# Kernel tuning notes

Measured on AMD Instinct MI355X. Metric: run time of the kernel, lower is better.

Reference implementation:

```python
import jax, jax.numpy as jnp
import numpy as np

N_NODES = 100000
N_EDGES = 1600000
IN_DIM, H1, H2, N_CLASSES = 128, 64, 64, 16
NEG_SLOPE = 0.2  # PyG GATConv default leaky_relu slope


def _xavier(key, shape, gain=1.414):
    fan_in, fan_out = shape[0], shape[-1]
    a = gain * np.sqrt(6.0 / (fan_in + fan_out))
    return jax.random.uniform(key, shape, jnp.float32, -a, a)


def setup_inputs() -> dict:
    key = jax.random.key(0)
    ks = jax.random.split(key, 12)
    ft_list = jax.random.normal(ks[0], (N_NODES, IN_DIM), jnp.float32)
    adj_tensor = jax.random.randint(ks[1], (2, N_EDGES), 0, N_NODES, jnp.int64)
    return {
        "ft_list": ft_list,
        "adj_tensor": adj_tensor,
        "W1": _xavier(ks[2], (IN_DIM, H1)),
        "a_src1": _xavier(ks[3], (H1, 1))[:, 0],
        "a_dst1": _xavier(ks[4], (H1, 1))[:, 0],
        "b1": jnp.zeros((H1,), jnp.float32),
        "W2": _xavier(ks[5], (H1, H2)),
        "a_src2": _xavier(ks[6], (H2, 1))[:, 0],
        "a_dst2": _xavier(ks[7], (H2, 1))[:, 0],
        "b2": jnp.zeros((H2,), jnp.float32),
        "clas_W": _xavier(ks[8], (H2, N_CLASSES)),
        "clas_b": _xavier(ks[9], (1, N_CLASSES)),
    }


def _gat_conv(x, src, dst, n, W, a_src, a_dst, b):
    # h: [N, H] transformed node features
    h = x @ W
    alpha_s = h @ a_src  # [N]
    alpha_d = h @ a_dst  # [N]
    # per-edge attention logit (gather)
    e = jax.nn.leaky_relu(alpha_s[src] + alpha_d[dst], NEG_SLOPE)  # [E]
    # segment softmax over edges grouped by destination node
    m = jax.ops.segment_max(e, dst, num_segments=n)
    p = jnp.exp(e - m[dst])
    s = jax.ops.segment_sum(p, dst, num_segments=n)
    attn = p / s[dst]  # [E]
    # weighted scatter-add of source features
    out = jax.ops.segment_sum(h[src] * attn[:, None], dst, num_segments=n)
    return out + b


def reference(ft_list, adj_tensor, W1, a_src1, a_dst1, b1, W2, a_src2, a_dst2, b2, clas_W, clas_b):
    n = ft_list.shape[0]
    loop = jnp.arange(n, dtype=adj_tensor.dtype)
    src = jnp.concatenate([adj_tensor[0], loop])  # add self-loops (PyG default)
    dst = jnp.concatenate([adj_tensor[1], loop])
    x = _gat_conv(ft_list, src, dst, n, W1, a_src1, a_dst1, b1)
    x = jax.nn.elu(x)
    # dropout(0.5) is identity in eval mode
    x = _gat_conv(x, src, dst, n, W2, a_src2, a_dst2, b2)
    logits = x @ clas_W + clas_b
    return logits, x
```

## Files before the change

### kernel.cpp

```cpp
#include <hip/hip_runtime.h>
#include <hip/hip_bf16.h>

#define NEG_SLOPE 0.2f
#define LOG2E 1.4426950408889634f
#define BSH 9
#define BW  (1 << BSH)
#define CH  4096
#define PGRID 256

typedef short short8 __attribute__((ext_vector_type(8)));
typedef float f32x4 __attribute__((ext_vector_type(4)));


__global__ __launch_bounds__(256) void bucket_hist_kernel(
    const int* __restrict__ adj, int* __restrict__ H, int E, int N, int R, int NBK)
{
    __shared__ int hist[256];
    const int t = threadIdx.x;
    const int ET = E + N;
    for (int r = blockIdx.x; r < R; r += gridDim.x) {
        hist[t] = 0;
        __syncthreads();
        int base = r * CH;
        for (int i = 0; i < CH / 256; ++i) {
            int e = base + i * 256 + t;
            if (e >= ET) break;
            int d = (e < E) ? adj[E + e] : (e - E);
            atomicAdd(&hist[d >> BSH], 1);
        }
        __syncthreads();
        if (t < NBK) H[r * NBK + t] = hist[t];
        __syncthreads();
    }
}

__global__ __launch_bounds__(256) void scan_rounds_kernel(
    const int* __restrict__ H, int* __restrict__ S2, int* __restrict__ tot,
    int R, int NBK)
{
    __shared__ int part[256];
    const int b = blockIdx.x;
    const int t = threadIdx.x;
    const int C = (R + 255) / 256;
    int r0 = t * C, r1 = min(R, r0 + C);
    int s = 0;
    for (int r = r0; r < r1; ++r) s += H[r * NBK + b];
    part[t] = s;
    __syncthreads();
    for (int off = 1; off < 256; off <<= 1) {
        int v = (t >= off) ? part[t - off] : 0;
        __syncthreads();
        part[t] += v;
        __syncthreads();
    }
    int run = (t > 0) ? part[t - 1] : 0;
    for (int r = r0; r < r1; ++r) {
        int h = H[r * NBK + b];
        S2[r * NBK + b] = run;
        run += h;
    }
    if (t == 255) tot[b] = part[255];
}

__global__ __launch_bounds__(256) void scan_tot_kernel(
    const int* __restrict__ tot, int* __restrict__ base, int NBK)
{
    __shared__ int s[256];
    int t = threadIdx.x;
    int v = (t < NBK) ? tot[t] : 0;
    s[t] = v;
    __syncthreads();
    for (int off = 1; off < 256; off <<= 1) {
        int u = (t >= off) ? s[t - off] : 0;
        __syncthreads();
        s[t] += u;
        __syncthreads();
    }
    if (t < NBK) base[t] = s[t] - v;
}

__global__ __launch_bounds__(256) void partition_kernel(
    const int* __restrict__ adj, const int* __restrict__ S2,
    const int* __restrict__ base, int* __restrict__ pbuf,
    int E, int N, int R, int NBK)
{
    __shared__ int lcur[256];
    const int t = threadIdx.x;
    const int ET = E + N;
    for (int r = blockIdx.x; r < R; r += gridDim.x) {
        if (t < NBK) lcur[t] = base[t] + S2[r * NBK + t];
        __syncthreads();
        int b0 = r * CH;
        for (int i = 0; i < CH / 256; ++i) {
            int e = b0 + i * 256 + t;
            if (e >= ET) break;
            int s, d;
            if (e < E) { d = adj[E + e]; s = adj[e]; }
            else       { s = d = e - E; }
            int b = d >> BSH;
            int pos = atomicAdd(&lcur[b], 1);
            pbuf[pos] = (s << BSH) | (d & (BW - 1));
        }
        __syncthreads();
    }
}

__global__ __launch_bounds__(256) void csr_build_kernel(
    const int* __restrict__ base, const int* __restrict__ tot,
    const int* __restrict__ pbuf,
    int* __restrict__ row_ptr, int* __restrict__ col_idx, int E, int N, int NBK)
{
    __shared__ int offA[BW];
    __shared__ int lcur[BW];
    const int b = blockIdx.x;
    const int t = threadIdx.x;
    const int node0 = b << BSH;
    const int nn = min(BW, N - node0);
    const int ET = E + N;
    const int segbeg = base[b];
    const int segend = segbeg + tot[b];

    offA[t] = 0; offA[t + 256] = 0;
    __syncthreads();
    for (int i = segbeg + t; i < segend; i += 256)
        atomicAdd(&offA[pbuf[i] & (BW - 1)], 1);
    __syncthreads();
    for (int off = 1; off < BW; off <<= 1) {
        int i1 = t + 256;
        int v0 = (t >= off) ? offA[t - off] : 0;
        int v1 = (i1 >= off) ? offA[i1 - off] : 0;
        __syncthreads();
        offA[t] += v0; offA[i1] += v1;
        __syncthreads();
    }
    if (t < nn) {
        int ex = t ? offA[t - 1] : 0;
        row_ptr[node0 + t] = segbeg + ex;
        lcur[t] = segbeg + ex;
    }
    int i2 = t + 256;
    if (i2 < nn) {
        int ex = offA[i2 - 1];
        row_ptr[node0 + i2] = segbeg + ex;
        lcur[i2] = segbeg + ex;
    }
    if (b == NBK - 1 && t == 0) row_ptr[N] = ET;
    __syncthreads();
    for (int i = segbeg + t; i < segend; i += 256) {
        int p = pbuf[i];
        int pos = atomicAdd(&lcur[p & (BW - 1)], 1);
        col_idx[pos] = p >> BSH;
    }
}


__device__ __forceinline__ unsigned short f2bf(float f)
{
    union { __hip_bfloat16 b; unsigned short u; } v;
    v.b = __float2bfloat16(f);
    return v.u;
}

__global__ __launch_bounds__(256) void prep_wfrag_kernel(
    const float* __restrict__ W, unsigned short* __restrict__ wf, int K)
{
    int total = K * 64;
    int idx = blockIdx.x * 256 + threadIdx.x;
    if (idx >= total) return;
    int i = idx & 7;
    int l = (idx >> 3) & 63;
    int f = idx >> 9;
    int s = f >> 2, tt = f & 3;
    int k = 32 * s + 8 * (l >> 4) + i;
    int n = 16 * tt + (l & 15);
    wf[idx] = f2bf(W[k * 64 + n]);
}

template<int K>
__global__ __launch_bounds__(256) void gemm_alpha_mfma(
    const float* __restrict__ X, const unsigned short* __restrict__ wf,
    const float* __restrict__ a_src, const float* __restrict__ a_dst,
    __hip_bfloat16* __restrict__ h, float* __restrict__ as_, float* __restrict__ ad_,
    int N, int nChunks)
{
    constexpr int S = K / 32;
    const int t = threadIdx.x;
    const int wave = t >> 6, lane = t & 63;
    const int g = lane >> 4, c = lane & 15;

    short8 bf[S * 4];
#pragma unroll
    for (int f = 0; f < S * 4; ++f)
        bf[f] = *(const short8*)(wf + ((size_t)(f * 64 + lane)) * 8);

    float asr[4], adr[4];
#pragma unroll
    for (int tt = 0; tt < 4; ++tt) {
        asr[tt] = a_src[16 * tt + c];
        adr[tt] = a_dst[16 * tt + c];
    }

    for (int chunk = blockIdx.x; chunk < nChunks; chunk += gridDim.x) {
        const int r0 = chunk * 64 + wave * 16;
        const int arow = r0 + c;
        const bool rv = arow < N;
        const float* xr = X + (size_t)arow * K;

        f32x4 acc[4];
#pragma unroll
        for (int tt = 0; tt < 4; ++tt) acc[tt] = (f32x4){0.f, 0.f, 0.f, 0.f};

#pragma unroll
        for (int s = 0; s < S; ++s) {
            float4 x0 = make_float4(0.f, 0.f, 0.f, 0.f);
            float4 x1 = make_float4(0.f, 0.f, 0.f, 0.f);
            if (rv) {
                const float4* p = (const float4*)(xr + 32 * s + 8 * g);
                x0 = p[0]; x1 = p[1];
            }
            float xs[8] = {x0.x, x0.y, x0.z, x0.w, x1.x, x1.y, x1.z, x1.w};
            union { short8 v; unsigned u[4]; } ah, al;
#pragma unroll
            for (int p2 = 0; p2 < 4; ++p2) {
                unsigned u0 = __float_as_uint(xs[2 * p2]);
                unsigned u1 = __float_as_uint(xs[2 * p2 + 1]);
                ah.u[p2] = (u0 >> 16) | (u1 & 0xffff0000u);
                float h0 = __uint_as_float(u0 & 0xffff0000u);
                float h1 = __uint_as_float(u1 & 0xffff0000u);
                unsigned l0 = __float_as_uint(xs[2 * p2] - h0);
                unsigned l1 = __float_as_uint(xs[2 * p2 + 1] - h1);
                al.u[p2] = (l0 >> 16) | (l1 & 0xffff0000u);
            }
#pragma unroll
            for (int tt = 0; tt < 4; ++tt) {
                acc[tt] = __builtin_amdgcn_mfma_f32_16x16x32_bf16(
                    ah.v, bf[s * 4 + tt], acc[tt], 0, 0, 0);
                acc[tt] = __builtin_amdgcn_mfma_f32_16x16x32_bf16(
                    al.v, bf[s * 4 + tt], acc[tt], 0, 0, 0);
            }
        }

#pragma unroll
        for (int i = 0; i < 4; ++i) {
            const int ri = r0 + 4 * g + i;
            float va = 0.f, vd = 0.f;
#pragma unroll
            for (int tt = 0; tt < 4; ++tt) {
                float v = acc[tt][i];
                va += v * asr[tt];
                vd += v * adr[tt];
                if (ri < N) h[(size_t)ri * 64 + 16 * tt + c] = __float2bfloat16(v);
            }
#pragma unroll
            for (int off = 8; off >= 1; off >>= 1) {
                va += __shfl_xor(va, off, 16);
                vd += __shfl_xor(vd, off, 16);
            }
            if (c == 0 && ri < N) { as_[ri] = va * LOG2E; ad_[ri] = vd * LOG2E; }
        }
    }
}

__global__ __launch_bounds__(256) void gat_aggregate_kernel(
    const int* __restrict__ row_ptr, const int* __restrict__ col_idx,
    const float* __restrict__ as_, const float* __restrict__ ad_,
    const __hip_bfloat16* __restrict__ h, const float* __restrict__ b,
    float* __restrict__ out, int N, int do_elu)
{
    int node = blockIdx.x * 4 + (threadIdx.x >> 6);
    int lane = threadIdx.x & 63;
    int sub = lane >> 3, q = lane & 7;
    if (node >= N) return;
    int beg = row_ptr[node], end = row_ptr[node + 1];
    float ad = ad_[node];
    float acc[8] = {0.f, 0.f, 0.f, 0.f, 0.f, 0.f, 0.f, 0.f};
    float psum = 0.f;

    const char* cbp = (const char*)col_idx;
    const char* abp = (const char*)as_;
    const char* hbp = (const char*)h;
    const unsigned qb = (unsigned)q * 16u;

    int base = beg;
    unsigned co = (unsigned)(beg + sub) * 4u;
    for (; base + 16 <= end; base += 16, co += 64u) {
        int s0 = *(const int*)(cbp + co);
        int s1 = *(const int*)(cbp + (co + 32u));
        float x0 = *(const float*)(abp + ((unsigned)s0 << 2)) + ad;
        float x1 = *(const float*)(abp + ((unsigned)s1 << 2)) + ad;
        uint4 u0 = *(const uint4*)(hbp + (((unsigned)s0 << 7) + qb));
        uint4 u1 = *(const uint4*)(hbp + (((unsigned)s1 << 7) + qb));
        x0 = fmaxf(x0, NEG_SLOPE * x0);
        x1 = fmaxf(x1, NEG_SLOPE * x1);
        float p0 = __builtin_amdgcn_exp2f(x0);
        float p1 = __builtin_amdgcn_exp2f(x1);
        psum += p0 + p1;
        unsigned w;
        w = u0.x; acc[0] += p0 * __uint_as_float(w << 16); acc[1] += p0 * __uint_as_float(w & 0xffff0000u);
        w = u0.y; acc[2] += p0 * __uint_as_float(w << 16); acc[3] += p0 * __uint_as_float(w & 0xffff0000u);
        w = u0.z; acc[4] += p0 * __uint_as_float(w << 16); acc[5] += p0 * __uint_as_float(w & 0xffff0000u);
        w = u0.w; acc[6] += p0 * __uint_as_float(w << 16); acc[7] += p0 * __uint_as_float(w & 0xffff0000u);
        w = u1.x; acc[0] += p1 * __uint_as_float(w << 16); acc[1] += p1 * __uint_as_float(w & 0xffff0000u);
        w = u1.y; acc[2] += p1 * __uint_as_float(w << 16); acc[3] += p1 * __uint_as_float(w & 0xffff0000u);
        w = u1.z; acc[4] += p1 * __uint_as_float(w << 16); acc[5] += p1 * __uint_as_float(w & 0xffff0000u);
        w = u1.w; acc[6] += p1 * __uint_as_float(w << 16); acc[7] += p1 * __uint_as_float(w & 0xffff0000u);
    }
    for (; base < end; base += 8, co += 32u) {
        int e0 = base + sub;
        bool v0 = e0 < end;
        unsigned c0 = (unsigned)(v0 ? e0 : end - 1) * 4u;
        int s0 = *(const int*)(cbp + c0);
        float x0 = *(const float*)(abp + ((unsigned)s0 << 2)) + ad;
        uint4 u0 = *(const uint4*)(hbp + (((unsigned)s0 << 7) + qb));
        x0 = fmaxf(x0, NEG_SLOPE * x0);
        float p0 = v0 ? __builtin_amdgcn_exp2f(x0) : 0.f;
        psum += p0;
        unsigned w;
        w = u0.x; acc[0] += p0 * __uint_as_float(w << 16); acc[1] += p0 * __uint_as_float(w & 0xffff0000u);
        w = u0.y; acc[2] += p0 * __uint_as_float(w << 16); acc[3] += p0 * __uint_as_float(w & 0xffff0000u);
        w = u0.z; acc[4] += p0 * __uint_as_float(w << 16); acc[5] += p0 * __uint_as_float(w & 0xffff0000u);
        w = u0.w; acc[6] += p0 * __uint_as_float(w << 16); acc[7] += p0 * __uint_as_float(w & 0xffff0000u);
    }
#pragma unroll
    for (int off = 8; off <= 32; off <<= 1) {
        psum += __shfl_xor(psum, off, 64);
#pragma unroll
        for (int j = 0; j < 8; ++j) acc[j] += __shfl_xor(acc[j], off, 64);
    }
    if (sub == 0) {
        float inv = 1.f / psum;
        const float* bq = b + q * 8;
        float4 b0 = *(const float4*)bq;
        float4 b1 = *(const float4*)(bq + 4);
        float v[8];
        v[0] = acc[0] * inv + b0.x; v[1] = acc[1] * inv + b0.y;
        v[2] = acc[2] * inv + b0.z; v[3] = acc[3] * inv + b0.w;
        v[4] = acc[4] * inv + b1.x; v[5] = acc[5] * inv + b1.y;
        v[6] = acc[6] * inv + b1.z; v[7] = acc[7] * inv + b1.w;
        if (do_elu) {
#pragma unroll
            for (int j = 0; j < 8; ++j)
                v[j] = v[j] > 0.f ? v[j] : (__expf(v[j]) - 1.f);
        }
        float* op = out + (size_t)node * 64 + q * 8;
        ((float4*)op)[0] = make_float4(v[0], v[1], v[2], v[3]);
        ((float4*)op)[1] = make_float4(v[4], v[5], v[6], v[7]);
    }
}

__global__ __launch_bounds__(256) void classifier_kernel(
    const float* __restrict__ x, const float* __restrict__ cw,
    const float* __restrict__ cb, float* __restrict__ out, int N)
{
    int i = blockIdx.x * blockDim.x + threadIdx.x;
    if (i >= N * 16) return;
    int n = i >> 4, c = i & 15;
    const float4* xr = (const float4*)(x + (size_t)n * 64);
    float acc = cb[c];
#pragma unroll
    for (int j4 = 0; j4 < 16; ++j4) {
        float4 xv = xr[j4];
        acc += xv.x * cw[(j4 * 4 + 0) * 16 + c];
        acc += xv.y * cw[(j4 * 4 + 1) * 16 + c];
        acc += xv.z * cw[(j4 * 4 + 2) * 16 + c];
        acc += xv.w * cw[(j4 * 4 + 3) * 16 + c];
    }
    out[i] = acc;
}

extern "C" void kernel_launch(void* const* d_in, const int* in_sizes, int n_in,
                              void* d_out, int out_size, void* d_ws, size_t ws_size,
                              hipStream_t stream)
{
    const float* X    = (const float*)d_in[0];
    const int*   adj  = (const int*)d_in[1];
    const float* W1   = (const float*)d_in[2];
    const float* a_s1 = (const float*)d_in[3];
    const float* a_d1 = (const float*)d_in[4];
    const float* b1   = (const float*)d_in[5];
    const float* W2   = (const float*)d_in[6];
    const float* a_s2 = (const float*)d_in[7];
    const float* a_d2 = (const float*)d_in[8];
    const float* b2   = (const float*)d_in[9];
    const float* cW   = (const float*)d_in[10];
    const float* cb   = (const float*)d_in[11];

    const int N   = in_sizes[0] / 128;
    const int E   = in_sizes[1] / 2;
    const int ET  = E + N;
    const int R   = (ET + CH - 1) / CH;
    const int NBK = (N + BW - 1) >> BSH;

    __hip_bfloat16* A = (__hip_bfloat16*)d_ws;
    float* B       = (float*)(A + (size_t)N * 64);
    float* asb     = B + (size_t)N * 64;
    float* adb     = asb + N;
    int*   row_ptr = (int*)(adb + N);
    int*   col_idx = row_ptr + (N + 1);
    int*   pbuf    = col_idx + ET;
    int*   H       = pbuf + ET;
    int*   S2      = H + R * NBK;
    int*   tot     = S2 + R * NBK;
    int*   base    = tot + NBK;

    uintptr_t wp = ((uintptr_t)pbuf + 15) & ~(uintptr_t)15;
    unsigned short* wf1 = (unsigned short*)wp;
    unsigned short* wf2 = wf1 + 128 * 64;

    const int T = 256;
    const int aggBlocks  = (N + 3) / 4;
    const int nChunks    = (N + 63) / 64;
    const int gemmBlocks = nChunks < 512 ? nChunks : 512;

    bucket_hist_kernel<<<PGRID, T, 0, stream>>>(adj, H, E, N, R, NBK);
    scan_rounds_kernel<<<NBK, T, 0, stream>>>(H, S2, tot, R, NBK);
    scan_tot_kernel<<<1, T, 0, stream>>>(tot, base, NBK);
    partition_kernel<<<PGRID, T, 0, stream>>>(adj, S2, base, pbuf, E, N, R, NBK);
    csr_build_kernel<<<NBK, T, 0, stream>>>(base, tot, pbuf, row_ptr, col_idx, E, N, NBK);

    prep_wfrag_kernel<<<(128 * 64 + 255) / 256, T, 0, stream>>>(W1, wf1, 128);
    prep_wfrag_kernel<<<(64 * 64 + 255) / 256, T, 0, stream>>>(W2, wf2, 64);

    gemm_alpha_mfma<128><<<gemmBlocks, T, 0, stream>>>(
        X, wf1, a_s1, a_d1, A, asb, adb, N, nChunks);
    gat_aggregate_kernel<<<aggBlocks, T, 0, stream>>>(
        row_ptr, col_idx, asb, adb, A, b1, B, N, 1);

    float* out  = (float*)d_out;
    float* xout = out + (size_t)N * 16;
    gemm_alpha_mfma<64><<<gemmBlocks, T, 0, stream>>>(
        B, wf2, a_s2, a_d2, A, asb, adb, N, nChunks);
    gat_aggregate_kernel<<<aggBlocks, T, 0, stream>>>(
        row_ptr, col_idx, asb, adb, A, b2, xout, N, 0);

    classifier_kernel<<<(N * 16 + T - 1) / T, T, 0, stream>>>(
        xout, cW, cb, out, N);
}
```

Measured before the change: 312.3 us.

## Map eight nodes per wave in GAT aggregation, removing cross-lane reductions

The aggregation kernel used to give each node a full 64-lane wave, with 8 sub-groups splitting that node's edges and a shuffle reduction at the end. Now each 8-lane sub-group owns one node and walks its edge list sequentially, two edges per iteration with a predicated tail. This drops the shuffle reduction and makes better use of lanes for low-degree nodes (about 17 edges on average). The cost is load imbalance across the nodes sharing a wave and a longer serial dependency chain per node.

```diff
diff --git a/kernel.cpp b/kernel.cpp
--- a/kernel.cpp
+++ b/kernel.cpp
@@ -267,12 +267,12 @@
     const __hip_bfloat16* __restrict__ h, const float* __restrict__ b,
     float* __restrict__ out, int N, int do_elu)
 {
-    int node = blockIdx.x * 4 + (threadIdx.x >> 6);
-    int lane = threadIdx.x & 63;
-    int sub = lane >> 3, q = lane & 7;
+    const int wave = threadIdx.x >> 6, lane = threadIdx.x & 63;
+    const int sub = lane >> 3, q = lane & 7;
+    const int node = blockIdx.x * 32 + wave * 8 + sub;
     if (node >= N) return;
-    int beg = row_ptr[node], end = row_ptr[node + 1];
-    float ad = ad_[node];
+    const int beg = row_ptr[node], end = row_ptr[node + 1];
+    const float ad = ad_[node];
     float acc[8] = {0.f, 0.f, 0.f, 0.f, 0.f, 0.f, 0.f, 0.f};
     float psum = 0.f;
 
@@ -281,11 +281,11 @@
     const char* hbp = (const char*)h;
     const unsigned qb = (unsigned)q * 16u;
 
-    int base = beg;
-    unsigned co = (unsigned)(beg + sub) * 4u;
-    for (; base + 16 <= end; base += 16, co += 64u) {
+    unsigned co = (unsigned)beg * 4u;
+    for (int i = beg; i < end; i += 2, co += 8u) {
+        const bool v1 = (i + 1) < end;
         int s0 = *(const int*)(cbp + co);
-        int s1 = *(const int*)(cbp + (co + 32u));
+        int s1 = *(const int*)(cbp + (v1 ? co + 4u : co));
         float x0 = *(const float*)(abp + ((unsigned)s0 << 2)) + ad;
         float x1 = *(const float*)(abp + ((unsigned)s1 << 2)) + ad;
         uint4 u0 = *(const uint4*)(hbp + (((unsigned)s0 << 7) + qb));
@@ -293,7 +293,7 @@
         x0 = fmaxf(x0, NEG_SLOPE * x0);
         x1 = fmaxf(x1, NEG_SLOPE * x1);
         float p0 = __builtin_amdgcn_exp2f(x0);
-        float p1 = __builtin_amdgcn_exp2f(x1);
+        float p1 = v1 ? __builtin_amdgcn_exp2f(x1) : 0.f;
         psum += p0 + p1;
         unsigned w;
         w = u0.x; acc[0] += p0 * __uint_as_float(w << 16); acc[1] += p0 * __uint_as_float(w & 0xffff0000u);
@@ -305,47 +305,24 @@
         w = u1.z; acc[4] += p1 * __uint_as_float(w << 16); acc[5] += p1 * __uint_as_float(w & 0xffff0000u);
         w = u1.w; acc[6] += p1 * __uint_as_float(w << 16); acc[7] += p1 * __uint_as_float(w & 0xffff0000u);
     }
-    for (; base < end; base += 8, co += 32u) {
-        int e0 = base + sub;
-        bool v0 = e0 < end;
-        unsigned c0 = (unsigned)(v0 ? e0 : end - 1) * 4u;
-        int s0 = *(const int*)(cbp + c0);
-        float x0 = *(const float*)(abp + ((unsigned)s0 << 2)) + ad;
-        uint4 u0 = *(const uint4*)(hbp + (((unsigned)s0 << 7) + qb));
-        x0 = fmaxf(x0, NEG_SLOPE * x0);
-        float p0 = v0 ? __builtin_amdgcn_exp2f(x0) : 0.f;
-        psum += p0;
-        unsigned w;
-        w = u0.x; acc[0] += p0 * __uint_as_float(w << 16); acc[1] += p0 * __uint_as_float(w & 0xffff0000u);
-        w = u0.y; acc[2] += p0 * __uint_as_float(w << 16); acc[3] += p0 * __uint_as_float(w & 0xffff0000u);
-        w = u0.z; acc[4] += p0 * __uint_as_float(w << 16); acc[5] += p0 * __uint_as_float(w & 0xffff0000u);
-        w = u0.w; acc[6] += p0 * __uint_as_float(w << 16); acc[7] += p0 * __uint_as_float(w & 0xffff0000u);
-    }
-#pragma unroll
-    for (int off = 8; off <= 32; off <<= 1) {
-        psum += __shfl_xor(psum, off, 64);
-#pragma unroll
-        for (int j = 0; j < 8; ++j) acc[j] += __shfl_xor(acc[j], off, 64);
-    }
-    if (sub == 0) {
-        float inv = 1.f / psum;
-        const float* bq = b + q * 8;
-        float4 b0 = *(const float4*)bq;
-        float4 b1 = *(const float4*)(bq + 4);
-        float v[8];
-        v[0] = acc[0] * inv + b0.x; v[1] = acc[1] * inv + b0.y;
-        v[2] = acc[2] * inv + b0.z; v[3] = acc[3] * inv + b0.w;
-        v[4] = acc[4] * inv + b1.x; v[5] = acc[5] * inv + b1.y;
-        v[6] = acc[6] * inv + b1.z; v[7] = acc[7] * inv + b1.w;
-        if (do_elu) {
-#pragma unroll
-            for (int j = 0; j < 8; ++j)
-                v[j] = v[j] > 0.f ? v[j] : (__expf(v[j]) - 1.f);
-        }
-        float* op = out + (size_t)node * 64 + q * 8;
-        ((float4*)op)[0] = make_float4(v[0], v[1], v[2], v[3]);
-        ((float4*)op)[1] = make_float4(v[4], v[5], v[6], v[7]);
-    }
+
+    const float inv = 1.f / psum;
+    const float* bq = b + q * 8;
+    float4 b0 = *(const float4*)bq;
+    float4 b1 = *(const float4*)(bq + 4);
+    float v[8];
+    v[0] = acc[0] * inv + b0.x; v[1] = acc[1] * inv + b0.y;
+    v[2] = acc[2] * inv + b0.z; v[3] = acc[3] * inv + b0.w;
+    v[4] = acc[4] * inv + b1.x; v[5] = acc[5] * inv + b1.y;
+    v[6] = acc[6] * inv + b1.z; v[7] = acc[7] * inv + b1.w;
+    if (do_elu) {
+#pragma unroll
+        for (int j = 0; j < 8; ++j)
+            v[j] = v[j] > 0.f ? v[j] : (__expf(v[j]) - 1.f);
+    }
+    float* op = out + (size_t)node * 64 + q * 8;
+    ((float4*)op)[0] = make_float4(v[0], v[1], v[2], v[3]);
+    ((float4*)op)[1] = make_float4(v[4], v[5], v[6], v[7]);
 }
 
 __global__ __launch_bounds__(256) void classifier_kernel(
@@ -408,7 +385,7 @@
     unsigned short* wf2 = wf1 + 128 * 64;
 
     const int T = 256;
-    const int aggBlocks  = (N + 3) / 4;
+    const int aggBlocks  = (N + 31) / 32;
     const int nChunks    = (N + 63) / 64;
     const int gemmBlocks = nChunks < 512 ? nChunks : 512;
 
```

Result: faster. 299.6 us (-4.1%).
